# Kernel optimization log

Measured on AMD Instinct MI355X. Metric: run time of the kernel, lower is better.

Reference implementation:

```python
import jax, jax.numpy as jnp
import numpy as np

ALPHA = 0.2
SIGMA_REC = 0.15
B, T, N, IN, OUT, MASK_LEN = 256, 750, 512, 6, 2, 250


def setup_inputs() -> dict:
    key = jax.random.key(0)
    k_u, k_noise, k_rec, k_in, k_out, k_mask = jax.random.split(key, 6)
    noise_scale = np.sqrt(2.0 * ALPHA * SIGMA_REC ** 2).astype(np.float32)
    return {
        "u": jax.random.normal(k_u, (B, T, IN), dtype=jnp.float32),
        "noise": noise_scale * jax.random.normal(k_noise, (B, T, N), dtype=jnp.float32),
        "w_rec": jax.random.normal(k_rec, (N, N), dtype=jnp.float32) / np.float32(np.sqrt(N)),
        "w_in": jax.random.normal(k_in, (N, IN), dtype=jnp.float32) / np.float32(np.sqrt(IN)),
        "w_out": jax.random.normal(k_out, (OUT, N), dtype=jnp.float32) / np.float32(np.sqrt(N)),
        "mask": jnp.sort(jax.random.randint(k_mask, (MASK_LEN,), 0, T)),
    }


def _run_rnn(u, noise, w_rec, w_in):
    # u: [B,T,IN], noise: [B,T,N]; leaky ReLU RNN, t-1 update steps.
    b, t, _ = u.shape
    n = w_rec.shape[0]
    # Precompute input drive for all steps: [T-1, B, N]
    drive = jnp.einsum('bti,ni->tbn', u[:, : t - 1], w_in) + jnp.swapaxes(noise[:, : t - 1], 0, 1)

    def step(h, d):
        h_new = (1.0 - ALPHA) * h + ALPHA * jax.nn.relu(h @ w_rec.T + d)
        return h_new, h_new

    h0 = jnp.zeros((b, n), dtype=u.dtype)
    _, hs = jax.lax.scan(step, h0, drive)            # [T-1, B, N]
    states = jnp.concatenate([h0[None], hs], axis=0)  # [T, B, N]
    return jnp.swapaxes(states, 0, 1)                 # [B, T, N]


def reference(u, noise, w_rec, w_in, w_out, mask):
    states = _run_rnn(u, noise, w_rec, w_in)
    out = jnp.einsum('btn,on->bto', states, w_out)  # output_layer(states)
    return states, out[:, mask, :], out
```

## Files before the change

### kernel.cpp

```cpp
#include <hip/hip_runtime.h>
#include <hip/hip_bf16.h>


typedef __attribute__((ext_vector_type(4))) float f32x4;
typedef __attribute__((ext_vector_type(8))) short s16x8;

constexpr int BB = 256, TT = 750, NN = 512, INN = 6, OUTN = 2, MLEN = 250;
constexpr int BBLK = 16;
constexpr int NBLKS = BB / BBLK;
constexpr int WPB = 8;
constexpr int NSL = NN / WPB;
constexpr int NREG = 47;
constexpr int NLDS = 64 - NREG;
constexpr int HBYTES = BBLK * NN * 2;
constexpr int WOFF = HBYTES;
constexpr int SMEM_BYTES = WOFF + WPB * NLDS * 1024;
constexpr int DRVELTS = NBLKS * WPB * 64 * 16;

__device__ __forceinline__ unsigned short f2bf(float f) {
    unsigned v = __float_as_uint(f);
    v += 0x7fffu + ((v >> 16) & 1u);
    return (unsigned short)(v >> 16);
}
__device__ __forceinline__ float bf2f(unsigned short h) {
    return __uint_as_float(((unsigned)h) << 16);
}

__global__ __launch_bounds__(256)
void drive_kernel(const float* __restrict__ u, const float* __restrict__ noise,
                  const float* __restrict__ w_in, unsigned short* __restrict__ drv)
{
    int gid = blockIdx.x * 256 + threadIdx.x;
    int t = gid >> 13;
    if (t >= TT - 1) return;
    int lane = gid & 63, w = (gid >> 6) & 7, blk = (gid >> 9) & 15;
    int qq = lane >> 4, lr = lane & 15;

    float wv[4][INN];
    #pragma unroll
    for (int tt = 0; tt < 4; ++tt) {
        int n = w * NSL + 16 * tt + lr;
        #pragma unroll
        for (int i = 0; i < INN; ++i) wv[tt][i] = w_in[n * INN + i];
    }
    alignas(16) unsigned short o[16];
    #pragma unroll
    for (int r = 0; r < 4; ++r) {
        int b = blk * BBLK + 4 * qq + r;
        const float* up = u + ((size_t)b * TT + t) * INN;
        float uv[INN];
        #pragma unroll
        for (int i = 0; i < INN; ++i) uv[i] = up[i];
        const float* np = noise + ((size_t)b * TT + t) * NN;
        #pragma unroll
        for (int tt = 0; tt < 4; ++tt) {
            int n = w * NSL + 16 * tt + lr;
            float d = np[n];
            #pragma unroll
            for (int i = 0; i < INN; ++i) d += uv[i] * wv[tt][i];
            o[tt * 4 + r] = f2bf(d);
        }
    }
    s16x8* dst = (s16x8*)(drv + (size_t)gid * 16);
    dst[0] = *(const s16x8*)&o[0];
    dst[1] = *(const s16x8*)&o[8];
}

__global__ __launch_bounds__(512, 2)
void rnn_scan_kernel(const float* __restrict__ w_rec,
                     const unsigned short* __restrict__ drv,
                     float* __restrict__ states)
{
    extern __shared__ char smem[];
    const int tid = threadIdx.x;
    const int w = tid >> 6, lane = tid & 63;
    const int qq = lane >> 4, lr = lane & 15, p7 = lr & 7;
    const int blk = blockIdx.x;
    const int bg = blk * BBLK;

    s16x8 breg[NREG];
    #pragma unroll
    for (int tt = 0; tt < 4; ++tt) {
        #pragma unroll
        for (int kk = 0; kk < 16; ++kk) {
            const int f = tt * 16 + kk;
            const int n = w * NSL + 16 * tt + lr;
            const float* p = w_rec + (size_t)n * NN + 32 * kk + 8 * qq;
            f32x4 x0 = *(const f32x4*)p;
            f32x4 x1 = *(const f32x4*)(p + 4);
            union { s16x8 v; unsigned short s[8]; } fr;
            #pragma unroll
            for (int j = 0; j < 4; ++j) { fr.s[j] = f2bf(x0[j]); fr.s[4+j] = f2bf(x1[j]); }
            if (f < NREG) breg[f] = fr.v;
            else *(s16x8*)(smem + WOFF + (w * NLDS + (f - NREG)) * 1024 + lane * 16) = fr.v;
        }
    }
    for (int i = tid; i < HBYTES / 4; i += 512) ((unsigned*)smem)[i] = 0u;
    for (int i = tid; i < BBLK * NN; i += 512)
        states[(size_t)(bg + (i >> 9)) * TT * NN + (i & 511)] = 0.f;
    __syncthreads();

    float stl[16];
    #pragma unroll
    for (int i = 0; i < 16; ++i) stl[i] = 0.f;

    const int rb64 = (p7 & 4) << 4;
    const int hbase0 = lr * 1024 + ((qq ^ (p7 & 3)) << 4);
    const char* hbE = smem + hbase0 + rb64;
    const char* hbO = smem + hbase0 - rb64;
    const char* wbase = smem + WOFF + w * (NLDS * 1024) + lane * 16;

    const int s0 = 8 * w + (lr >> 3);
    const unsigned LB = 4096u * qq + ((unsigned)(s0 ^ (4 * (qq & 1))) << 4) + 2 * (lr & 7);

    float* rowp[4];
    #pragma unroll
    for (int r = 0; r < 4; ++r)
        rowp[r] = states + ((size_t)(bg + 4 * qq + r) * TT + 1) * NN + w * NSL + lr;

    const unsigned short* dptr = drv + ((size_t)(blk * WPB + w) * 64 + lane) * 16;

    for (int s = 1; s < TT; ++s) {
        const s16x8* dp = (const s16x8*)dptr;
        s16x8 dv0 = dp[0], dv1 = dp[1];
        dptr += DRVELTS;

        f32x4 a0 = {0.f,0.f,0.f,0.f}, a1 = a0, a2 = a0, a3 = a0;
        #pragma unroll
        for (int kk = 0; kk < 16; ++kk) {
            s16x8 av = *(const s16x8*)(((kk & 1) ? hbO : hbE) + (kk << 6));
            a0 = __builtin_amdgcn_mfma_f32_16x16x32_bf16(av, breg[kk],      a0, 0,0,0);
            a1 = __builtin_amdgcn_mfma_f32_16x16x32_bf16(av, breg[16 + kk], a1, 0,0,0);
            if (kk < 15)
                a2 = __builtin_amdgcn_mfma_f32_16x16x32_bf16(av, breg[32+kk], a2, 0,0,0);
            else
                a2 = __builtin_amdgcn_mfma_f32_16x16x32_bf16(
                         av, *(const s16x8*)wbase, a2, 0, 0, 0);
            a3 = __builtin_amdgcn_mfma_f32_16x16x32_bf16(
                     av, *(const s16x8*)(wbase + ((kk + 1) << 10)), a3, 0, 0, 0);
        }

        union { s16x8 v; unsigned short e[8]; } U0, U1;
        U0.v = dv0; U1.v = dv1;
        const f32x4 aX[4] = {a0, a1, a2, a3};
        float hnv[4][4];
        #pragma unroll
        for (int tt = 0; tt < 4; ++tt) {
            #pragma unroll
            for (int r = 0; r < 4; ++r) {
                float d = bf2f(tt < 2 ? U0.e[tt * 4 + r] : U1.e[(tt - 2) * 4 + r]);
                float pre = aX[tt][r] + d;
                float hn = 0.8f * stl[tt * 4 + r] + 0.2f * fmaxf(pre, 0.f);
                stl[tt * 4 + r] = hn;
                hnv[tt][r] = hn;
                __builtin_nontemporal_store(hn, rowp[r] + tt * 16);
            }
        }
        unsigned pk[8];
        #pragma unroll
        for (int p = 0; p < 2; ++p)
            #pragma unroll
            for (int r = 0; r < 4; ++r) {
                __hip_bfloat162 h2 = __float22bfloat162_rn(
                    make_float2(hnv[2 * p][r], hnv[2 * p + 1][r]));
                pk[p * 4 + r] = *reinterpret_cast<unsigned*>(&h2);
            }
        #pragma unroll
        for (int r = 0; r < 4; ++r) rowp[r] += NN;

        asm volatile("s_waitcnt lgkmcnt(0)\n\ts_barrier" ::: "memory");

        #pragma unroll
        for (int tt = 0; tt < 4; ++tt) {
            #pragma unroll
            for (int r = 0; r < 4; ++r) {
                const unsigned C = (unsigned)(((2 * tt) ^ r) << 4);
                unsigned short hv = (tt & 1) ? (unsigned short)(pk[(tt >> 1) * 4 + r] >> 16)
                                             : (unsigned short)(pk[(tt >> 1) * 4 + r]);
                *(unsigned short*)(smem + ((LB ^ C) + 1024 * r)) = hv;
            }
        }
        asm volatile("s_waitcnt lgkmcnt(0)\n\ts_barrier" ::: "memory");
    }
}

__global__ __launch_bounds__(256)
void proj_kernel(const float* __restrict__ states, const float* __restrict__ w_out,
                 float* __restrict__ outf)
{
    const int wv   = (blockIdx.x * blockDim.x + threadIdx.x) >> 6;
    const int lane = threadIdx.x & 63;
    const float* sp = states + (size_t)wv * NN + lane * 8;
    const float* w0 = w_out + lane * 8;
    const float* w1 = w_out + NN + lane * 8;
    float d0 = 0.f, d1 = 0.f;
    #pragma unroll
    for (int i = 0; i < 8; ++i) {
        float sv = sp[i];
        d0 += sv * w0[i];
        d1 += sv * w1[i];
    }
    #pragma unroll
    for (int off = 32; off > 0; off >>= 1) {
        d0 += __shfl_xor(d0, off);
        d1 += __shfl_xor(d1, off);
    }
    if (lane == 0) {
        outf[(size_t)wv * 2]     = d0;
        outf[(size_t)wv * 2 + 1] = d1;
    }
}

__global__ void mask_kernel(const int* __restrict__ mask, const float* __restrict__ outf,
                            float* __restrict__ outm)
{
    int idx = blockIdx.x * blockDim.x + threadIdx.x;
    if (idx >= BB * MLEN * OUTN) return;
    int o  = idx % OUTN;
    int jm = (idx / OUTN) % MLEN;
    int b  = idx / (OUTN * MLEN);
    int t  = mask[jm];
    outm[idx] = outf[((size_t)b * TT + t) * OUTN + o];
}

extern "C" void kernel_launch(void* const* d_in, const int* in_sizes, int n_in,
                              void* d_out, int out_size, void* d_ws, size_t ws_size,
                              hipStream_t stream)
{
    (void)in_sizes; (void)n_in; (void)out_size; (void)ws_size;
    const float* u     = (const float*)d_in[0];
    const float* noise = (const float*)d_in[1];
    const float* w_rec = (const float*)d_in[2];
    const float* w_in  = (const float*)d_in[3];
    const float* w_out = (const float*)d_in[4];
    const int*   mask  = (const int*)d_in[5];

    float* states = (float*)d_out;
    float* outm   = states + (size_t)BB * TT * NN;
    float* outf   = outm + (size_t)BB * MLEN * OUTN;

    unsigned short* drvpk = (unsigned short*)d_ws;

    hipFuncSetAttribute((const void*)rnn_scan_kernel,
                        hipFuncAttributeMaxDynamicSharedMemorySize, SMEM_BYTES);

    drive_kernel<<<(TT - 1) * 32, 256, 0, stream>>>(u, noise, w_in, drvpk);
    rnn_scan_kernel<<<NBLKS, 512, SMEM_BYTES, stream>>>(w_rec, drvpk, states);
    proj_kernel<<<(BB * TT) / 4, 256, 0, stream>>>(states, w_out, outf);
    mask_kernel<<<(BB * MLEN * OUTN + 255) / 256, 256, 0, stream>>>(mask, outf, outm);
}
```

Baseline: 2.110 ms.

## Double-buffer hidden state in LDS to drop one barrier per RNN step

Hidden state now ping-pongs between two LDS buffers, so each timestep writes the next state into the other buffer and needs only one barrier instead of two. The loop is unrolled by two via a macro that alternates buffers, MFMA sections are wrapped in s_setprio, and one more weight fragment per wave is kept in registers (48 instead of 47). This doubles the LDS used for hidden state and raises register pressure, which may affect occupancy or cause spills at two blocks per CU.

```diff
diff --git a/kernel.cpp b/kernel.cpp
--- a/kernel.cpp
+++ b/kernel.cpp
@@ -10,11 +10,12 @@
 constexpr int NBLKS = BB / BBLK;
 constexpr int WPB = 8;
 constexpr int NSL = NN / WPB;
-constexpr int NREG = 47;
-constexpr int NLDS = 64 - NREG;
-constexpr int HBYTES = BBLK * NN * 2;
-constexpr int WOFF = HBYTES;
-constexpr int SMEM_BYTES = WOFF + WPB * NLDS * 1024;
+constexpr int NREG = 48;
+constexpr int NLDS = 16;
+constexpr int HBUF = BBLK * NN * 2;
+constexpr int WOFF = 2 * HBUF;
+constexpr int WSTRIDE = NLDS * 1024;
+constexpr int SMEM_BYTES = WOFF + WPB * WSTRIDE;
 constexpr int DRVELTS = NBLKS * WPB * 64 * 16;
 
 __device__ __forceinline__ unsigned short f2bf(float f) {
@@ -65,6 +66,56 @@
     dst[0] = *(const s16x8*)&o[0];
     dst[1] = *(const s16x8*)&o[8];
 }
+
+#define STEP(RB, WB)                                                              \
+  {                                                                               \
+    const s16x8* dp = (const s16x8*)dptr;                                         \
+    s16x8 dv0 = dp[0], dv1 = dp[1];                                               \
+    dptr += DRVELTS;                                                              \
+    const char* hbE = hE##RB;                                                     \
+    const char* hbO = hO##RB;                                                     \
+    f32x4 a0 = {0.f,0.f,0.f,0.f}, a1 = a0, a2 = a0, a3 = a0;                      \
+    __builtin_amdgcn_s_setprio(1);                                                \
+    _Pragma("unroll")                                                             \
+    for (int kk = 0; kk < 16; ++kk) {                                             \
+      s16x8 av = *(const s16x8*)(((kk & 1) ? hbO : hbE) + (kk << 6));             \
+      a0 = __builtin_amdgcn_mfma_f32_16x16x32_bf16(av, breg[kk],      a0, 0,0,0); \
+      a1 = __builtin_amdgcn_mfma_f32_16x16x32_bf16(av, breg[16 + kk], a1, 0,0,0); \
+      a2 = __builtin_amdgcn_mfma_f32_16x16x32_bf16(av, breg[32 + kk], a2, 0,0,0); \
+      a3 = __builtin_amdgcn_mfma_f32_16x16x32_bf16(                               \
+               av, *(const s16x8*)(wbase + (kk << 10)), a3, 0, 0, 0);             \
+    }                                                                             \
+    __builtin_amdgcn_s_setprio(0);                                                \
+    union { s16x8 v; unsigned short e[8]; } U0, U1;                               \
+    U0.v = dv0; U1.v = dv1;                                                       \
+    char* bufc = smem + (WB) * HBUF;                                              \
+    _Pragma("unroll")                                                             \
+    for (int r = 0; r < 4; ++r) {                                                 \
+      float h0 = 0.8f * stl[0*4+r] + 0.2f * fmaxf(a0[r] + bf2f(U0.e[r]),     0.f);\
+      float h1 = 0.8f * stl[1*4+r] + 0.2f * fmaxf(a1[r] + bf2f(U0.e[4 + r]), 0.f);\
+      float h2 = 0.8f * stl[2*4+r] + 0.2f * fmaxf(a2[r] + bf2f(U1.e[r]),     0.f);\
+      float h3 = 0.8f * stl[3*4+r] + 0.2f * fmaxf(a3[r] + bf2f(U1.e[4 + r]), 0.f);\
+      stl[0*4+r] = h0; stl[1*4+r] = h1; stl[2*4+r] = h2; stl[3*4+r] = h3;         \
+      __builtin_nontemporal_store(h0, rowp[r] + 0);                               \
+      __builtin_nontemporal_store(h1, rowp[r] + 16);                              \
+      __builtin_nontemporal_store(h2, rowp[r] + 32);                              \
+      __builtin_nontemporal_store(h3, rowp[r] + 48);                              \
+      __hip_bfloat162 p01 = __float22bfloat162_rn(make_float2(h0, h1));           \
+      __hip_bfloat162 p23 = __float22bfloat162_rn(make_float2(h2, h3));           \
+      unsigned q01 = *reinterpret_cast<unsigned*>(&p01);                          \
+      unsigned q23 = *reinterpret_cast<unsigned*>(&p23);                          \
+      *(unsigned short*)(bufc + ((LB ^ (unsigned)((0 ^ r) << 4)) + 1024 * r))     \
+          = (unsigned short)q01;                                                  \
+      *(unsigned short*)(bufc + ((LB ^ (unsigned)((2 ^ r) << 4)) + 1024 * r))     \
+          = (unsigned short)(q01 >> 16);                                          \
+      *(unsigned short*)(bufc + ((LB ^ (unsigned)((4 ^ r) << 4)) + 1024 * r))     \
+          = (unsigned short)q23;                                                  \
+      *(unsigned short*)(bufc + ((LB ^ (unsigned)((6 ^ r) << 4)) + 1024 * r))     \
+          = (unsigned short)(q23 >> 16);                                          \
+      rowp[r] += NN;                                                              \
+    }                                                                             \
+    asm volatile("s_waitcnt lgkmcnt(0)\n\ts_barrier" ::: "memory");               \
+  }
 
 __global__ __launch_bounds__(512, 2)
 void rnn_scan_kernel(const float* __restrict__ w_rec,
@@ -92,10 +143,10 @@
             #pragma unroll
             for (int j = 0; j < 4; ++j) { fr.s[j] = f2bf(x0[j]); fr.s[4+j] = f2bf(x1[j]); }
             if (f < NREG) breg[f] = fr.v;
-            else *(s16x8*)(smem + WOFF + (w * NLDS + (f - NREG)) * 1024 + lane * 16) = fr.v;
+            else *(s16x8*)(smem + WOFF + w * WSTRIDE + (f - NREG) * 1024 + lane * 16) = fr.v;
         }
     }
-    for (int i = tid; i < HBYTES / 4; i += 512) ((unsigned*)smem)[i] = 0u;
+    for (int i = tid; i < WOFF / 4; i += 512) ((unsigned*)smem)[i] = 0u;
     for (int i = tid; i < BBLK * NN; i += 512)
         states[(size_t)(bg + (i >> 9)) * TT * NN + (i & 511)] = 0.f;
     __syncthreads();
@@ -106,9 +157,11 @@
 
     const int rb64 = (p7 & 4) << 4;
     const int hbase0 = lr * 1024 + ((qq ^ (p7 & 3)) << 4);
-    const char* hbE = smem + hbase0 + rb64;
-    const char* hbO = smem + hbase0 - rb64;
-    const char* wbase = smem + WOFF + w * (NLDS * 1024) + lane * 16;
+    const char* hE0 = smem + hbase0 + rb64;
+    const char* hO0 = smem + hbase0 - rb64;
+    const char* hE1 = hE0 + HBUF;
+    const char* hO1 = hO0 + HBUF;
+    const char* wbase = smem + WOFF + w * WSTRIDE + lane * 16;
 
     const int s0 = 8 * w + (lr >> 3);
     const unsigned LB = 4096u * qq + ((unsigned)(s0 ^ (4 * (qq & 1))) << 4) + 2 * (lr & 7);
@@ -120,68 +173,11 @@
 
     const unsigned short* dptr = drv + ((size_t)(blk * WPB + w) * 64 + lane) * 16;
 
-    for (int s = 1; s < TT; ++s) {
-        const s16x8* dp = (const s16x8*)dptr;
-        s16x8 dv0 = dp[0], dv1 = dp[1];
-        dptr += DRVELTS;
-
-        f32x4 a0 = {0.f,0.f,0.f,0.f}, a1 = a0, a2 = a0, a3 = a0;
-        #pragma unroll
-        for (int kk = 0; kk < 16; ++kk) {
-            s16x8 av = *(const s16x8*)(((kk & 1) ? hbO : hbE) + (kk << 6));
-            a0 = __builtin_amdgcn_mfma_f32_16x16x32_bf16(av, breg[kk],      a0, 0,0,0);
-            a1 = __builtin_amdgcn_mfma_f32_16x16x32_bf16(av, breg[16 + kk], a1, 0,0,0);
-            if (kk < 15)
-                a2 = __builtin_amdgcn_mfma_f32_16x16x32_bf16(av, breg[32+kk], a2, 0,0,0);
-            else
-                a2 = __builtin_amdgcn_mfma_f32_16x16x32_bf16(
-                         av, *(const s16x8*)wbase, a2, 0, 0, 0);
-            a3 = __builtin_amdgcn_mfma_f32_16x16x32_bf16(
-                     av, *(const s16x8*)(wbase + ((kk + 1) << 10)), a3, 0, 0, 0);
-        }
-
-        union { s16x8 v; unsigned short e[8]; } U0, U1;
-        U0.v = dv0; U1.v = dv1;
-        const f32x4 aX[4] = {a0, a1, a2, a3};
-        float hnv[4][4];
-        #pragma unroll
-        for (int tt = 0; tt < 4; ++tt) {
-            #pragma unroll
-            for (int r = 0; r < 4; ++r) {
-                float d = bf2f(tt < 2 ? U0.e[tt * 4 + r] : U1.e[(tt - 2) * 4 + r]);
-                float pre = aX[tt][r] + d;
-                float hn = 0.8f * stl[tt * 4 + r] + 0.2f * fmaxf(pre, 0.f);
-                stl[tt * 4 + r] = hn;
-                hnv[tt][r] = hn;
-                __builtin_nontemporal_store(hn, rowp[r] + tt * 16);
-            }
-        }
-        unsigned pk[8];
-        #pragma unroll
-        for (int p = 0; p < 2; ++p)
-            #pragma unroll
-            for (int r = 0; r < 4; ++r) {
-                __hip_bfloat162 h2 = __float22bfloat162_rn(
-                    make_float2(hnv[2 * p][r], hnv[2 * p + 1][r]));
-                pk[p * 4 + r] = *reinterpret_cast<unsigned*>(&h2);
-            }
-        #pragma unroll
-        for (int r = 0; r < 4; ++r) rowp[r] += NN;
-
-        asm volatile("s_waitcnt lgkmcnt(0)\n\ts_barrier" ::: "memory");
-
-        #pragma unroll
-        for (int tt = 0; tt < 4; ++tt) {
-            #pragma unroll
-            for (int r = 0; r < 4; ++r) {
-                const unsigned C = (unsigned)(((2 * tt) ^ r) << 4);
-                unsigned short hv = (tt & 1) ? (unsigned short)(pk[(tt >> 1) * 4 + r] >> 16)
-                                             : (unsigned short)(pk[(tt >> 1) * 4 + r]);
-                *(unsigned short*)(smem + ((LB ^ C) + 1024 * r)) = hv;
-            }
-        }
-        asm volatile("s_waitcnt lgkmcnt(0)\n\ts_barrier" ::: "memory");
-    }
+    for (int s = 1; s < TT - 1; s += 2) {
+        STEP(0, 1)
+        STEP(1, 0)
+    }
+    STEP(0, 1)
 }
 
 __global__ __launch_bounds__(256)
```

Result: slower. 2.248 ms (+6.6%).

## Split recurrent weight fragments across registers, LDS, and L2-resident global memory

Applied to the files above, without the earlier changes.

Recurrent weight fragments were held as 47 in registers and 17 in LDS. They are now split as 38 in registers, 17 in LDS and 9 in a pre-packed bf16 global buffer written by a new packB kernel. The 9 global fragments are reloaded every timestep in three batches, interleaved with the MFMA loop, and should hit in cache. This frees registers, likely to ease pressure or spilling, and spreads load traffic across the LDS and global paths. The elementwise epilogue is also fused so the state update, store and bf16 packing happen in one loop. The cost is global-load latency on the serial critical path of every step.

```diff
diff --git a/kernel.cpp b/kernel.cpp
--- a/kernel.cpp
+++ b/kernel.cpp
@@ -10,12 +10,14 @@
 constexpr int NBLKS = BB / BBLK;
 constexpr int WPB = 8;
 constexpr int NSL = NN / WPB;
-constexpr int NREG = 47;
-constexpr int NLDS = 64 - NREG;
+constexpr int NREG = 38;
+constexpr int NLDSF = 17;
+constexpr int NGLB = 9;
 constexpr int HBYTES = BBLK * NN * 2;
 constexpr int WOFF = HBYTES;
-constexpr int SMEM_BYTES = WOFF + WPB * NLDS * 1024;
+constexpr int SMEM_BYTES = WOFF + WPB * NLDSF * 1024;
 constexpr int DRVELTS = NBLKS * WPB * 64 * 16;
+constexpr size_t DRVTOT = (size_t)(TT - 1) * DRVELTS;
 
 __device__ __forceinline__ unsigned short f2bf(float f) {
     unsigned v = __float_as_uint(f);
@@ -66,9 +68,28 @@
     dst[1] = *(const s16x8*)&o[8];
 }
 
+__global__ __launch_bounds__(256)
+void packB_kernel(const float* __restrict__ w_rec, unsigned short* __restrict__ gB)
+{
+    int gid = blockIdx.x * 256 + threadIdx.x;
+    if (gid >= WPB * NGLB * 64) return;
+    int lane = gid & 63;
+    int rem  = gid >> 6;
+    int w = rem / NGLB, i = rem - w * NGLB;
+    int lr = lane & 15, qq = lane >> 4;
+    int n = 64 * w + 48 + lr;
+    int k = 32 * (7 + i) + 8 * qq;
+    const float* p = w_rec + (size_t)n * NN + k;
+    alignas(16) unsigned short o[8];
+    #pragma unroll
+    for (int j = 0; j < 8; ++j) o[j] = f2bf(p[j]);
+    *(s16x8*)(gB + (size_t)gid * 8) = *(const s16x8*)&o[0];
+}
+
 __global__ __launch_bounds__(512, 2)
 void rnn_scan_kernel(const float* __restrict__ w_rec,
                      const unsigned short* __restrict__ drv,
+                     const unsigned short* __restrict__ gB,
                      float* __restrict__ states)
 {
     extern __shared__ char smem[];
@@ -84,6 +105,7 @@
         #pragma unroll
         for (int kk = 0; kk < 16; ++kk) {
             const int f = tt * 16 + kk;
+            if (f >= NREG + NLDSF) continue;
             const int n = w * NSL + 16 * tt + lr;
             const float* p = w_rec + (size_t)n * NN + 32 * kk + 8 * qq;
             f32x4 x0 = *(const f32x4*)p;
@@ -92,7 +114,7 @@
             #pragma unroll
             for (int j = 0; j < 4; ++j) { fr.s[j] = f2bf(x0[j]); fr.s[4+j] = f2bf(x1[j]); }
             if (f < NREG) breg[f] = fr.v;
-            else *(s16x8*)(smem + WOFF + (w * NLDS + (f - NREG)) * 1024 + lane * 16) = fr.v;
+            else *(s16x8*)(smem + WOFF + (w * NLDSF + (f - NREG)) * 1024 + lane * 16) = fr.v;
         }
     }
     for (int i = tid; i < HBYTES / 4; i += 512) ((unsigned*)smem)[i] = 0u;
@@ -108,7 +130,7 @@
     const int hbase0 = lr * 1024 + ((qq ^ (p7 & 3)) << 4);
     const char* hbE = smem + hbase0 + rb64;
     const char* hbO = smem + hbase0 - rb64;
-    const char* wbase = smem + WOFF + w * (NLDS * 1024) + lane * 16;
+    const char* wbase = smem + WOFF + w * (NLDSF * 1024) + lane * 16;
 
     const int s0 = 8 * w + (lr >> 3);
     const unsigned LB = 4096u * qq + ((unsigned)(s0 ^ (4 * (qq & 1))) << 4) + 2 * (lr & 7);
@@ -119,52 +141,69 @@
         rowp[r] = states + ((size_t)(bg + 4 * qq + r) * TT + 1) * NN + w * NSL + lr;
 
     const unsigned short* dptr = drv + ((size_t)(blk * WPB + w) * 64 + lane) * 16;
+    const char* gq = (const char*)gB + ((size_t)(w * NGLB) * 64 + lane) * 16;
 
     for (int s = 1; s < TT; ++s) {
+        asm volatile("" : "+v"(gq));
         const s16x8* dp = (const s16x8*)dptr;
         s16x8 dv0 = dp[0], dv1 = dp[1];
         dptr += DRVELTS;
 
         f32x4 a0 = {0.f,0.f,0.f,0.f}, a1 = a0, a2 = a0, a3 = a0;
+        s16x8 gb[NGLB];
+
         #pragma unroll
         for (int kk = 0; kk < 16; ++kk) {
+            if (kk == 0) {
+                gb[0] = *(const s16x8*)(gq);
+                gb[1] = *(const s16x8*)(gq + 1024);
+                gb[2] = *(const s16x8*)(gq + 2048);
+            }
+            if (kk == 4) {
+                gb[3] = *(const s16x8*)(gq + 3072);
+                gb[4] = *(const s16x8*)(gq + 4096);
+                gb[5] = *(const s16x8*)(gq + 5120);
+            }
+            if (kk == 8) {
+                gb[6] = *(const s16x8*)(gq + 6144);
+                gb[7] = *(const s16x8*)(gq + 7168);
+                gb[8] = *(const s16x8*)(gq + 8192);
+            }
             s16x8 av = *(const s16x8*)(((kk & 1) ? hbO : hbE) + (kk << 6));
             a0 = __builtin_amdgcn_mfma_f32_16x16x32_bf16(av, breg[kk],      a0, 0,0,0);
             a1 = __builtin_amdgcn_mfma_f32_16x16x32_bf16(av, breg[16 + kk], a1, 0,0,0);
-            if (kk < 15)
+            if (kk < 6)
                 a2 = __builtin_amdgcn_mfma_f32_16x16x32_bf16(av, breg[32+kk], a2, 0,0,0);
             else
                 a2 = __builtin_amdgcn_mfma_f32_16x16x32_bf16(
-                         av, *(const s16x8*)wbase, a2, 0, 0, 0);
-            a3 = __builtin_amdgcn_mfma_f32_16x16x32_bf16(
-                     av, *(const s16x8*)(wbase + ((kk + 1) << 10)), a3, 0, 0, 0);
+                         av, *(const s16x8*)(wbase + ((kk - 6) << 10)), a2, 0, 0, 0);
+            if (kk < 7)
+                a3 = __builtin_amdgcn_mfma_f32_16x16x32_bf16(
+                         av, *(const s16x8*)(wbase + ((10 + kk) << 10)), a3, 0, 0, 0);
+            else
+                a3 = __builtin_amdgcn_mfma_f32_16x16x32_bf16(av, gb[kk - 7], a3, 0,0,0);
         }
 
         union { s16x8 v; unsigned short e[8]; } U0, U1;
         U0.v = dv0; U1.v = dv1;
-        const f32x4 aX[4] = {a0, a1, a2, a3};
-        float hnv[4][4];
-        #pragma unroll
-        for (int tt = 0; tt < 4; ++tt) {
+        const f32x4 aP[4] = {a0, a1, a2, a3};
+        unsigned pk[8];
+        #pragma unroll
+        for (int p = 0; p < 2; ++p) {
             #pragma unroll
             for (int r = 0; r < 4; ++r) {
-                float d = bf2f(tt < 2 ? U0.e[tt * 4 + r] : U1.e[(tt - 2) * 4 + r]);
-                float pre = aX[tt][r] + d;
-                float hn = 0.8f * stl[tt * 4 + r] + 0.2f * fmaxf(pre, 0.f);
-                stl[tt * 4 + r] = hn;
-                hnv[tt][r] = hn;
-                __builtin_nontemporal_store(hn, rowp[r] + tt * 16);
-            }
-        }
-        unsigned pk[8];
-        #pragma unroll
-        for (int p = 0; p < 2; ++p)
-            #pragma unroll
-            for (int r = 0; r < 4; ++r) {
-                __hip_bfloat162 h2 = __float22bfloat162_rn(
-                    make_float2(hnv[2 * p][r], hnv[2 * p + 1][r]));
+                float dE = bf2f(p == 0 ? U0.e[r]     : U1.e[r]);
+                float dO = bf2f(p == 0 ? U0.e[4 + r] : U1.e[4 + r]);
+                float hE = 0.8f * stl[(2*p)*4 + r]   + 0.2f * fmaxf(aP[2*p][r]   + dE, 0.f);
+                float hO = 0.8f * stl[(2*p+1)*4 + r] + 0.2f * fmaxf(aP[2*p+1][r] + dO, 0.f);
+                stl[(2*p)*4 + r] = hE;
+                stl[(2*p+1)*4 + r] = hO;
+                __builtin_nontemporal_store(hE, rowp[r] + (2*p) * 16);
+                __builtin_nontemporal_store(hO, rowp[r] + (2*p+1) * 16);
+                __hip_bfloat162 h2 = __float22bfloat162_rn(make_float2(hE, hO));
                 pk[p * 4 + r] = *reinterpret_cast<unsigned*>(&h2);
             }
+        }
         #pragma unroll
         for (int r = 0; r < 4; ++r) rowp[r] += NN;
 
@@ -240,12 +279,14 @@
     float* outf   = outm + (size_t)BB * MLEN * OUTN;
 
     unsigned short* drvpk = (unsigned short*)d_ws;
+    unsigned short* gB    = drvpk + DRVTOT;
 
     hipFuncSetAttribute((const void*)rnn_scan_kernel,
                         hipFuncAttributeMaxDynamicSharedMemorySize, SMEM_BYTES);
 
     drive_kernel<<<(TT - 1) * 32, 256, 0, stream>>>(u, noise, w_in, drvpk);
-    rnn_scan_kernel<<<NBLKS, 512, SMEM_BYTES, stream>>>(w_rec, drvpk, states);
+    packB_kernel<<<(WPB * NGLB * 64 + 255) / 256, 256, 0, stream>>>(w_rec, gB);
+    rnn_scan_kernel<<<NBLKS, 512, SMEM_BYTES, stream>>>(w_rec, drvpk, gB, states);
     proj_kernel<<<(BB * TT) / 4, 256, 0, stream>>>(states, w_out, outf);
     mask_kernel<<<(BB * MLEN * OUTN + 255) / 256, 256, 0, stream>>>(mask, outf, outm);
 }
```

Measured after the change: 2.536 ms. 1.2x slower.

## Halve scan workgroup to 4 waves, each computing 8 column tiles

Applied to the files above, without the earlier changes.

The recurrent scan kernel now runs 4 waves per block instead of 8. Each wave owns 128 output columns (8 MFMA tiles), keeps 92 weight fragments in registers and spills the remaining 36 to LDS, and the drive kernel's data layout is remapped to match. The carried hidden state is now held as packed bf16 instead of fp32, which frees registers but makes the leaky-integration recurrence accumulate bf16 rounding error. The intent is to lower per-step barrier and synchronisation cost by using fewer waves, in exchange for more serial MFMA work per wave and heavier register pressure.

```diff
diff --git a/kernel.cpp b/kernel.cpp
--- a/kernel.cpp
+++ b/kernel.cpp
@@ -8,14 +8,14 @@
 constexpr int BB = 256, TT = 750, NN = 512, INN = 6, OUTN = 2, MLEN = 250;
 constexpr int BBLK = 16;
 constexpr int NBLKS = BB / BBLK;
-constexpr int WPB = 8;
+constexpr int WPB = 4;
 constexpr int NSL = NN / WPB;
-constexpr int NREG = 47;
-constexpr int NLDS = 64 - NREG;
+constexpr int NREG = 92;
+constexpr int NLDSF = 36;
 constexpr int HBYTES = BBLK * NN * 2;
 constexpr int WOFF = HBYTES;
-constexpr int SMEM_BYTES = WOFF + WPB * NLDS * 1024;
-constexpr int DRVELTS = NBLKS * WPB * 64 * 16;
+constexpr int SMEM_BYTES = WOFF + WPB * NLDSF * 1024;
+constexpr int DRVELTS = NBLKS * WPB * 2 * 64 * 16;
 
 __device__ __forceinline__ unsigned short f2bf(float f) {
     unsigned v = __float_as_uint(f);
@@ -33,15 +33,15 @@
     int gid = blockIdx.x * 256 + threadIdx.x;
     int t = gid >> 13;
     if (t >= TT - 1) return;
-    int lane = gid & 63, w = (gid >> 6) & 7, blk = (gid >> 9) & 15;
+    int lane = gid & 63, p = (gid >> 6) & 1, w = (gid >> 7) & 3, blk = (gid >> 9) & 15;
     int qq = lane >> 4, lr = lane & 15;
 
     float wv[4][INN];
     #pragma unroll
-    for (int tt = 0; tt < 4; ++tt) {
-        int n = w * NSL + 16 * tt + lr;
-        #pragma unroll
-        for (int i = 0; i < INN; ++i) wv[tt][i] = w_in[n * INN + i];
+    for (int tl = 0; tl < 4; ++tl) {
+        int n = w * NSL + 16 * (4 * p + tl) + lr;
+        #pragma unroll
+        for (int i = 0; i < INN; ++i) wv[tl][i] = w_in[n * INN + i];
     }
     alignas(16) unsigned short o[16];
     #pragma unroll
@@ -53,12 +53,12 @@
         for (int i = 0; i < INN; ++i) uv[i] = up[i];
         const float* np = noise + ((size_t)b * TT + t) * NN;
         #pragma unroll
-        for (int tt = 0; tt < 4; ++tt) {
-            int n = w * NSL + 16 * tt + lr;
+        for (int tl = 0; tl < 4; ++tl) {
+            int n = w * NSL + 16 * (4 * p + tl) + lr;
             float d = np[n];
             #pragma unroll
-            for (int i = 0; i < INN; ++i) d += uv[i] * wv[tt][i];
-            o[tt * 4 + r] = f2bf(d);
+            for (int i = 0; i < INN; ++i) d += uv[i] * wv[tl][i];
+            o[tl * 4 + r] = f2bf(d);
         }
     }
     s16x8* dst = (s16x8*)(drv + (size_t)gid * 16);
@@ -66,7 +66,7 @@
     dst[1] = *(const s16x8*)&o[8];
 }
 
-__global__ __launch_bounds__(512, 2)
+__global__ __launch_bounds__(256, 1)
 void rnn_scan_kernel(const float* __restrict__ w_rec,
                      const unsigned short* __restrict__ drv,
                      float* __restrict__ states)
@@ -80,11 +80,11 @@
 
     s16x8 breg[NREG];
     #pragma unroll
-    for (int tt = 0; tt < 4; ++tt) {
+    for (int ttn = 0; ttn < 8; ++ttn) {
         #pragma unroll
         for (int kk = 0; kk < 16; ++kk) {
-            const int f = tt * 16 + kk;
-            const int n = w * NSL + 16 * tt + lr;
+            const int f = ttn * 16 + kk;
+            const int n = w * NSL + 16 * ttn + lr;
             const float* p = w_rec + (size_t)n * NN + 32 * kk + 8 * qq;
             f32x4 x0 = *(const f32x4*)p;
             f32x4 x1 = *(const f32x4*)(p + 4);
@@ -92,25 +92,25 @@
             #pragma unroll
             for (int j = 0; j < 4; ++j) { fr.s[j] = f2bf(x0[j]); fr.s[4+j] = f2bf(x1[j]); }
             if (f < NREG) breg[f] = fr.v;
-            else *(s16x8*)(smem + WOFF + (w * NLDS + (f - NREG)) * 1024 + lane * 16) = fr.v;
-        }
-    }
-    for (int i = tid; i < HBYTES / 4; i += 512) ((unsigned*)smem)[i] = 0u;
-    for (int i = tid; i < BBLK * NN; i += 512)
+            else *(s16x8*)(smem + WOFF + (w * NLDSF + (f - NREG)) * 1024 + lane * 16) = fr.v;
+        }
+    }
+    for (int i = tid; i < HBYTES / 4; i += 256) ((unsigned*)smem)[i] = 0u;
+    for (int i = tid; i < BBLK * NN; i += 256)
         states[(size_t)(bg + (i >> 9)) * TT * NN + (i & 511)] = 0.f;
     __syncthreads();
 
-    float stl[16];
-    #pragma unroll
-    for (int i = 0; i < 16; ++i) stl[i] = 0.f;
+    unsigned pkS[16];
+    #pragma unroll
+    for (int i = 0; i < 16; ++i) pkS[i] = 0u;
 
     const int rb64 = (p7 & 4) << 4;
     const int hbase0 = lr * 1024 + ((qq ^ (p7 & 3)) << 4);
     const char* hbE = smem + hbase0 + rb64;
     const char* hbO = smem + hbase0 - rb64;
-    const char* wbase = smem + WOFF + w * (NLDS * 1024) + lane * 16;
-
-    const int s0 = 8 * w + (lr >> 3);
+    const char* wbase = smem + WOFF + w * (NLDSF * 1024) + lane * 16;
+
+    const int s0 = 16 * w + (lr >> 3);
     const unsigned LB = 4096u * qq + ((unsigned)(s0 ^ (4 * (qq & 1))) << 4) + 2 * (lr & 7);
 
     float* rowp[4];
@@ -118,65 +118,70 @@
     for (int r = 0; r < 4; ++r)
         rowp[r] = states + ((size_t)(bg + 4 * qq + r) * TT + 1) * NN + w * NSL + lr;
 
-    const unsigned short* dptr = drv + ((size_t)(blk * WPB + w) * 64 + lane) * 16;
+    const unsigned short* dptr = drv + ((size_t)(blk * WPB + w) * 2) * 1024 + lane * 16;
 
     for (int s = 1; s < TT; ++s) {
-        const s16x8* dp = (const s16x8*)dptr;
-        s16x8 dv0 = dp[0], dv1 = dp[1];
+        const s16x8* dp0 = (const s16x8*)dptr;
+        const s16x8* dp1 = (const s16x8*)(dptr + 1024);
+        s16x8 dv00 = dp0[0], dv01 = dp0[1];
+        s16x8 dv10 = dp1[0], dv11 = dp1[1];
         dptr += DRVELTS;
 
-        f32x4 a0 = {0.f,0.f,0.f,0.f}, a1 = a0, a2 = a0, a3 = a0;
+        f32x4 acc[8];
+        #pragma unroll
+        for (int i = 0; i < 8; ++i) acc[i] = f32x4{0.f, 0.f, 0.f, 0.f};
+
         #pragma unroll
         for (int kk = 0; kk < 16; ++kk) {
             s16x8 av = *(const s16x8*)(((kk & 1) ? hbO : hbE) + (kk << 6));
-            a0 = __builtin_amdgcn_mfma_f32_16x16x32_bf16(av, breg[kk],      a0, 0,0,0);
-            a1 = __builtin_amdgcn_mfma_f32_16x16x32_bf16(av, breg[16 + kk], a1, 0,0,0);
-            if (kk < 15)
-                a2 = __builtin_amdgcn_mfma_f32_16x16x32_bf16(av, breg[32+kk], a2, 0,0,0);
-            else
-                a2 = __builtin_amdgcn_mfma_f32_16x16x32_bf16(
-                         av, *(const s16x8*)wbase, a2, 0, 0, 0);
-            a3 = __builtin_amdgcn_mfma_f32_16x16x32_bf16(
-                     av, *(const s16x8*)(wbase + ((kk + 1) << 10)), a3, 0, 0, 0);
-        }
-
-        union { s16x8 v; unsigned short e[8]; } U0, U1;
-        U0.v = dv0; U1.v = dv1;
-        const f32x4 aX[4] = {a0, a1, a2, a3};
-        float hnv[4][4];
-        #pragma unroll
-        for (int tt = 0; tt < 4; ++tt) {
+            #pragma unroll
+            for (int ttn = 0; ttn < 8; ++ttn) {
+                const int f = ttn * 16 + kk;
+                s16x8 bv = (f < NREG)
+                    ? breg[f]
+                    : *(const s16x8*)(wbase + ((f - NREG) << 10));
+                acc[ttn] = __builtin_amdgcn_mfma_f32_16x16x32_bf16(av, bv, acc[ttn], 0, 0, 0);
+            }
+        }
+
+        union Vu { s16x8 v; unsigned short e[8]; };
+        Vu d00, d01, d10, d11;
+        d00.v = dv00; d01.v = dv01; d10.v = dv10; d11.v = dv11;
+        #pragma unroll
+        for (int q = 0; q < 4; ++q) {
+            const int ttE = 2 * q, ttO = 2 * q + 1;
             #pragma unroll
             for (int r = 0; r < 4; ++r) {
-                float d = bf2f(tt < 2 ? U0.e[tt * 4 + r] : U1.e[(tt - 2) * 4 + r]);
-                float pre = aX[tt][r] + d;
-                float hn = 0.8f * stl[tt * 4 + r] + 0.2f * fmaxf(pre, 0.f);
-                stl[tt * 4 + r] = hn;
-                hnv[tt][r] = hn;
-                __builtin_nontemporal_store(hn, rowp[r] + tt * 16);
+                const int eE = (ttE & 3) * 4 + r;
+                const int eO = (ttO & 3) * 4 + r;
+                float dE = bf2f((ttE < 4) ? (eE < 8 ? d00.e[eE] : d01.e[eE - 8])
+                                          : (eE < 8 ? d10.e[eE] : d11.e[eE - 8]));
+                float dO = bf2f((ttO < 4) ? (eO < 8 ? d00.e[eO] : d01.e[eO - 8])
+                                          : (eO < 8 ? d10.e[eO] : d11.e[eO - 8]));
+                const unsigned ps = pkS[q * 4 + r];
+                float hpE = bf2f((unsigned short)ps);
+                float hpO = bf2f((unsigned short)(ps >> 16));
+                float hE = 0.8f * hpE + 0.2f * fmaxf(acc[ttE][r] + dE, 0.f);
+                float hO = 0.8f * hpO + 0.2f * fmaxf(acc[ttO][r] + dO, 0.f);
+                __builtin_nontemporal_store(hE, rowp[r] + ttE * 16);
+                __builtin_nontemporal_store(hO, rowp[r] + ttO * 16);
+                __hip_bfloat162 h2 = __float22bfloat162_rn(make_float2(hE, hO));
+                pkS[q * 4 + r] = *reinterpret_cast<unsigned*>(&h2);
             }
         }
-        unsigned pk[8];
-        #pragma unroll
-        for (int p = 0; p < 2; ++p)
+        #pragma unroll
+        for (int r = 0; r < 4; ++r) rowp[r] += NN;
+
+        asm volatile("s_waitcnt lgkmcnt(0)\n\ts_barrier" ::: "memory");
+
+        #pragma unroll
+        for (int ttn = 0; ttn < 8; ++ttn) {
             #pragma unroll
             for (int r = 0; r < 4; ++r) {
-                __hip_bfloat162 h2 = __float22bfloat162_rn(
-                    make_float2(hnv[2 * p][r], hnv[2 * p + 1][r]));
-                pk[p * 4 + r] = *reinterpret_cast<unsigned*>(&h2);
-            }
-        #pragma unroll
-        for (int r = 0; r < 4; ++r) rowp[r] += NN;
-
-        asm volatile("s_waitcnt lgkmcnt(0)\n\ts_barrier" ::: "memory");
-
-        #pragma unroll
-        for (int tt = 0; tt < 4; ++tt) {
-            #pragma unroll
-            for (int r = 0; r < 4; ++r) {
-                const unsigned C = (unsigned)(((2 * tt) ^ r) << 4);
-                unsigned short hv = (tt & 1) ? (unsigned short)(pk[(tt >> 1) * 4 + r] >> 16)
-                                             : (unsigned short)(pk[(tt >> 1) * 4 + r]);
+                const unsigned C = (unsigned)(((2 * ttn) ^ r) << 4);
+                const unsigned v = pkS[(ttn >> 1) * 4 + r];
+                unsigned short hv = (ttn & 1) ? (unsigned short)(v >> 16)
+                                              : (unsigned short)v;
                 *(unsigned short*)(smem + ((LB ^ C) + 1024 * r)) = hv;
             }
         }
@@ -245,7 +250,7 @@
                         hipFuncAttributeMaxDynamicSharedMemorySize, SMEM_BYTES);
 
     drive_kernel<<<(TT - 1) * 32, 256, 0, stream>>>(u, noise, w_in, drvpk);
-    rnn_scan_kernel<<<NBLKS, 512, SMEM_BYTES, stream>>>(w_rec, drvpk, states);
+    rnn_scan_kernel<<<NBLKS, 256, SMEM_BYTES, stream>>>(w_rec, drvpk, states);
     proj_kernel<<<(BB * TT) / 4, 256, 0, stream>>>(states, w_out, outf);
     mask_kernel<<<(BB * MLEN * OUTN + 255) / 256, 256, 0, stream>>>(mask, outf, outm);
 }
```

After: 2.933 ms. 39.0% more time.
